# Kernel tuning notes

Hardware: AMD Instinct MI355X
Metric: run time of the kernel (lower is better)

Reference implementation:

```python
import jax, jax.numpy as jnp
import numpy as np

QMIN, QMAX = 0.0, 255.0  # uint8 affine quantization range


def _quant_dequant(x, scale, zero_point):
    # affine static quantization: q = clamp(round(x/scale) + zp, 0, 255)
    q = jnp.clip(jnp.round(x / scale) + zero_point, QMIN, QMAX)
    # dequantize back to float for the reference GEMM
    return (q - zero_point) * scale


def setup_inputs() -> dict:
    key = jax.random.key(0)
    k1, k2, k3, k4, k5 = jax.random.split(key, 5)
    N, IN, OUT = 4096, 4096, 4096
    x = jax.random.normal(k1, (N, IN), dtype=jnp.float32)
    weight = jax.random.normal(k2, (OUT, IN), dtype=jnp.float32) * 0.02
    bias = jax.random.normal(k3, (OUT,), dtype=jnp.float32)
    # static qparams (as produced by calculate_qparams of the observers)
    act_scale = jnp.float32(4.0 * 2.0 / 255.0)  # covers ~[-4, 4]
    act_zero_point = jnp.int32(128)
    weight_scale = (jax.random.uniform(k4, (OUT,), dtype=jnp.float32) * 0.5 + 0.5) * (0.08 * 2.0 / 255.0)
    weight_zero_point = jnp.full((OUT,), 128, dtype=jnp.int32)
    return {
        "x": x,
        "weight": weight,
        "bias": bias,
        "act_scale": act_scale,
        "act_zero_point": act_zero_point,
        "weight_scale": weight_scale,
        "weight_zero_point": weight_zero_point,
    }


def reference(x, weight, bias, act_scale, act_zero_point, weight_scale, weight_zero_point):
    # per-tensor static activation quantization
    x_dq = _quant_dequant(x, act_scale, act_zero_point.astype(jnp.float32))  # [N, in]
    # per-output-row weight quantization (block_size = (1, in_features))
    w_dq = _quant_dequant(
        weight,
        weight_scale[:, None],
        weight_zero_point.astype(jnp.float32)[:, None],
    )  # [out, in]
    # F.linear: x @ W^T + b
    return jnp.einsum("ni,oi->no", x_dq, w_dq) + bias
```

## Files before the change

### kernel.cpp

```cpp
#include <hip/hip_runtime.h>
#include <stdint.h>

typedef int   int4v   __attribute__((ext_vector_type(4)));
typedef float float4v __attribute__((ext_vector_type(4)));

static constexpr int DIM = 4096;
static constexpr int BM  = 256, BN = 256;
static constexpr int BK  = 128;
static constexpr int NKT = DIM / BK;

__global__ __launch_bounds__(256) void quant_act_kernel(
    const float* __restrict__ x, const float* __restrict__ s_ptr,
    const int* __restrict__ zp_ptr, int* __restrict__ out, int n4) {
  const float s  = s_ptr[0];
  const int   zp = zp_ptr[0];
  int idx    = blockIdx.x * blockDim.x + threadIdx.x;
  int stride = gridDim.x * blockDim.x;
  for (int i = idx; i < n4; i += stride) {
    float4v v = reinterpret_cast<const float4v*>(x)[i];
    int packed = 0;
#pragma unroll
    for (int j = 0; j < 4; ++j) {
      int q = (int)rintf(v[j] / s) + zp;
      q = min(max(q, 0), 255);
      q -= zp;
      packed |= (q & 255) << (8 * j);
    }
    out[i] = packed;
  }
}

__global__ __launch_bounds__(256) void quant_wgt_kernel(
    const float* __restrict__ w, const float* __restrict__ ws,
    const int* __restrict__ wzp, int* __restrict__ out, int n4) {
  int idx    = blockIdx.x * blockDim.x + threadIdx.x;
  int stride = gridDim.x * blockDim.x;
  for (int i = idx; i < n4; i += stride) {
    const int row = i >> 10;
    const float s = ws[row];
    const int  zp = wzp[row];
    float4v v = reinterpret_cast<const float4v*>(w)[i];
    int packed = 0;
#pragma unroll
    for (int j = 0; j < 4; ++j) {
      int q = (int)rintf(v[j] / s) + zp;
      q = min(max(q, 0), 255);
      q -= zp;
      packed |= (q & 255) << (8 * j);
    }
    out[i] = packed;
  }
}


#define PHASE_MFMA(MH, NH)                                                    \
  __builtin_amdgcn_s_barrier();                                               \
  asm volatile("s_waitcnt lgkmcnt(0)" ::: "memory");                          \
  __builtin_amdgcn_s_setprio(1);                                              \
  _Pragma("unroll") for (int kk = 0; kk < 2; ++kk)                            \
  _Pragma("unroll") for (int m = 0; m < 4; ++m)                               \
  _Pragma("unroll") for (int n = 0; n < 2; ++n)                               \
      acc[(MH)*4 + m][(NH)*2 + n] = __builtin_amdgcn_mfma_i32_16x16x64_i8(    \
          af[m][kk], bf[(NH)*2 + n][kk], acc[(MH)*4 + m][(NH)*2 + n], 0,0,0); \
  __builtin_amdgcn_s_setprio(0);                                              \
  __builtin_amdgcn_s_barrier();

__global__ __launch_bounds__(512) void gemm_i8_8ph(
    const signed char* __restrict__ A, const signed char* __restrict__ B,
    const float* __restrict__ s_act, const float* __restrict__ w_scale,
    const float* __restrict__ bias, float* __restrict__ C) {
  extern __shared__ signed char smem[];

  const int tid  = threadIdx.x;
  const int w    = tid >> 6;
  const int lane = tid & 63;
  const int wr = w >> 2, wc = w & 3;
  const int l15 = lane & 15, lhi = lane >> 4;
  const int swk = (l15 & 7) << 4;

  const int srow = lane >> 3;
  const int scol = ((lane & 7) ^ (lane >> 3)) << 4;

  const int tileM = blockIdx.y * BM;
  const int tileN = blockIdx.x * BN;

  auto stageA = [&](int i, int ktn, signed char* aL) {
    const int c = 4 * w + i;
    const size_t g = (size_t)(tileM + c * 8 + srow) * DIM + (size_t)ktn * BK + scol;
    __builtin_amdgcn_global_load_lds(
        (const __attribute__((address_space(1))) void*)(A + g),
        (__attribute__((address_space(3))) void*)(aL + c * 1024), 16, 0, 0);
  };
  auto stageB = [&](int i, int ktn, signed char* bL) {
    const int c = 4 * w + i;
    const size_t g = (size_t)(tileN + c * 8 + srow) * DIM + (size_t)ktn * BK + scol;
    __builtin_amdgcn_global_load_lds(
        (const __attribute__((address_space(1))) void*)(B + g),
        (__attribute__((address_space(3))) void*)(bL + c * 1024), 16, 0, 0);
  };
  auto rdA = [&](const signed char* aL, int mh, int m, int kk) -> int4v {
    const int r = wr * 128 + (mh * 4 + m) * 16 + l15;
    return *(const int4v*)(aL + r * BK + ((kk * 64 + lhi * 16) ^ swk));
  };
  auto rdB = [&](const signed char* bL, int nidx, int kk) -> int4v {
    const int r = wc * 64 + nidx * 16 + l15;
    return *(const int4v*)(bL + r * BK + ((kk * 64 + lhi * 16) ^ swk));
  };

  int4v acc[8][4] = {};
  int4v af[4][2];
  int4v bf[4][2];

  {
    signed char* aL = smem;
    signed char* bL = smem + 32768;
#pragma unroll
    for (int i = 0; i < 4; ++i) { stageA(i, 0, aL); stageB(i, 0, bL); }
  }
  asm volatile("s_waitcnt vmcnt(0)" ::: "memory");
  __builtin_amdgcn_s_barrier();

  for (int kt = 0; kt < NKT; ++kt) {
    signed char* aL = smem + (kt & 1) * 65536;
    signed char* bL = aL + 32768;
    signed char* aN = smem + ((kt + 1) & 1) * 65536;
    signed char* bN = aN + 32768;
    const int ktn = (kt + 1 < NKT) ? kt + 1 : kt;

#pragma unroll
    for (int m = 0; m < 4; ++m) { af[m][0] = rdA(aL, 0, m, 0); af[m][1] = rdA(aL, 0, m, 1); }
#pragma unroll
    for (int n = 0; n < 2; ++n) { bf[n][0] = rdB(bL, n, 0); bf[n][1] = rdB(bL, n, 1); }
    stageA(0, ktn, aN); stageA(1, ktn, aN); stageA(2, ktn, aN);
    PHASE_MFMA(0, 0)

#pragma unroll
    for (int n = 2; n < 4; ++n) { bf[n][0] = rdB(bL, n, 0); bf[n][1] = rdB(bL, n, 1); }
    stageA(3, ktn, aN); stageB(0, ktn, bN); stageB(1, ktn, bN);
    PHASE_MFMA(0, 1)

#pragma unroll
    for (int m = 0; m < 4; ++m) { af[m][0] = rdA(aL, 1, m, 0); af[m][1] = rdA(aL, 1, m, 1); }
    stageB(2, ktn, bN); stageB(3, ktn, bN);
    PHASE_MFMA(1, 0)

    __builtin_amdgcn_s_setprio(1);
#pragma unroll
    for (int kk = 0; kk < 2; ++kk)
#pragma unroll
      for (int m = 0; m < 4; ++m)
#pragma unroll
        for (int n = 0; n < 2; ++n)
          acc[4 + m][2 + n] = __builtin_amdgcn_mfma_i32_16x16x64_i8(
              af[m][kk], bf[2 + n][kk], acc[4 + m][2 + n], 0, 0, 0);
    __builtin_amdgcn_s_setprio(0);
    asm volatile("s_waitcnt vmcnt(0)" ::: "memory");
    __builtin_amdgcn_s_barrier();
  }

  const float sa = s_act[0];
#pragma unroll
  for (int n = 0; n < 4; ++n) {
    const int col = tileN + wc * 64 + n * 16 + l15;
    const float sc = sa * w_scale[col];
    const float bs = bias[col];
#pragma unroll
    for (int m = 0; m < 8; ++m) {
      const int rbase = tileM + wr * 128 + m * 16 + lhi * 4;
#pragma unroll
      for (int j = 0; j < 4; ++j)
        C[(size_t)(rbase + j) * DIM + col] = (float)acc[m][n][j] * sc + bs;
    }
  }
}

extern "C" void kernel_launch(void* const* d_in, const int* in_sizes, int n_in,
                              void* d_out, int out_size, void* d_ws, size_t ws_size,
                              hipStream_t stream) {
  const float* x    = (const float*)d_in[0];
  const float* w    = (const float*)d_in[1];
  const float* bias = (const float*)d_in[2];
  const float* a_s  = (const float*)d_in[3];
  const int*   a_zp = (const int*)d_in[4];
  const float* w_s  = (const float*)d_in[5];
  const int*   w_zp = (const int*)d_in[6];
  float* out = (float*)d_out;

  signed char* a8 = (signed char*)d_ws;
  signed char* b8 = a8 + (size_t)DIM * DIM;

  const int n4 = DIM * DIM / 4;
  quant_act_kernel<<<2048, 256, 0, stream>>>(x, a_s, a_zp, (int*)a8, n4);
  quant_wgt_kernel<<<2048, 256, 0, stream>>>(w, w_s, w_zp, (int*)b8, n4);

  (void)hipFuncSetAttribute((const void*)gemm_i8_8ph,
                            hipFuncAttributeMaxDynamicSharedMemorySize, 131072);
  dim3 grid(DIM / BN, DIM / BM);
  gemm_i8_8ph<<<grid, 512, 131072, stream>>>(a8, b8, a_s, w_s, bias, out);
}
```

Before: 97.28 us.

## Deepen GEMM global-to-LDS prefetch to two tiles and swizzle blocks across XCDs

The int8 GEMM now preloads two K tiles before the loop. It then refills the buffer just consumed with tile kt+2, waiting on vmcnt(8) instead of draining all loads. This gives global loads a full iteration of lead time to hide memory latency. The 2D grid becomes a 1D grid whose block index is remapped so that consecutive tiles of the same rows and columns land on the same XCD, which should improve L2 reuse of A and B. The refill is now issued in one burst after the third phase rather than spread across phases, which may cause bursty memory traffic.

```diff
diff --git a/kernel.cpp b/kernel.cpp
--- a/kernel.cpp
+++ b/kernel.cpp
@@ -81,8 +81,10 @@
   const int srow = lane >> 3;
   const int scol = ((lane & 7) ^ (lane >> 3)) << 4;
 
-  const int tileM = blockIdx.y * BM;
-  const int tileN = blockIdx.x * BN;
+  const int bid = blockIdx.x;
+  const int swz = (bid & 7) * 32 + (bid >> 3);
+  const int tileM = (swz >> 4) * BM;
+  const int tileN = (swz & 15) * BN;
 
   auto stageA = [&](int i, int ktn, signed char* aL) {
     const int c = 4 * w + i;
@@ -112,38 +114,41 @@
   int4v bf[4][2];
 
   {
-    signed char* aL = smem;
-    signed char* bL = smem + 32768;
-#pragma unroll
-    for (int i = 0; i < 4; ++i) { stageA(i, 0, aL); stageB(i, 0, bL); }
-  }
-  asm volatile("s_waitcnt vmcnt(0)" ::: "memory");
+    signed char* a0 = smem;
+    signed char* b0 = smem + 32768;
+    signed char* a1 = smem + 65536;
+    signed char* b1 = smem + 65536 + 32768;
+#pragma unroll
+    for (int i = 0; i < 4; ++i) { stageA(i, 0, a0); stageB(i, 0, b0); }
+#pragma unroll
+    for (int i = 0; i < 4; ++i) { stageA(i, 1, a1); stageB(i, 1, b1); }
+  }
+  asm volatile("s_waitcnt vmcnt(8)" ::: "memory");
   __builtin_amdgcn_s_barrier();
 
   for (int kt = 0; kt < NKT; ++kt) {
     signed char* aL = smem + (kt & 1) * 65536;
     signed char* bL = aL + 32768;
-    signed char* aN = smem + ((kt + 1) & 1) * 65536;
-    signed char* bN = aN + 32768;
-    const int ktn = (kt + 1 < NKT) ? kt + 1 : kt;
 
 #pragma unroll
     for (int m = 0; m < 4; ++m) { af[m][0] = rdA(aL, 0, m, 0); af[m][1] = rdA(aL, 0, m, 1); }
 #pragma unroll
     for (int n = 0; n < 2; ++n) { bf[n][0] = rdB(bL, n, 0); bf[n][1] = rdB(bL, n, 1); }
-    stageA(0, ktn, aN); stageA(1, ktn, aN); stageA(2, ktn, aN);
     PHASE_MFMA(0, 0)
 
 #pragma unroll
     for (int n = 2; n < 4; ++n) { bf[n][0] = rdB(bL, n, 0); bf[n][1] = rdB(bL, n, 1); }
-    stageA(3, ktn, aN); stageB(0, ktn, bN); stageB(1, ktn, bN);
     PHASE_MFMA(0, 1)
 
 #pragma unroll
     for (int m = 0; m < 4; ++m) { af[m][0] = rdA(aL, 1, m, 0); af[m][1] = rdA(aL, 1, m, 1); }
-    stageB(2, ktn, bN); stageB(3, ktn, bN);
     PHASE_MFMA(1, 0)
 
+    const bool st = (kt + 2 < NKT);
+    if (st) {
+#pragma unroll
+      for (int i = 0; i < 4; ++i) { stageA(i, kt + 2, aL); stageB(i, kt + 2, bL); }
+    }
     __builtin_amdgcn_s_setprio(1);
 #pragma unroll
     for (int kk = 0; kk < 2; ++kk)
@@ -154,7 +159,11 @@
           acc[4 + m][2 + n] = __builtin_amdgcn_mfma_i32_16x16x64_i8(
               af[m][kk], bf[2 + n][kk], acc[4 + m][2 + n], 0, 0, 0);
     __builtin_amdgcn_s_setprio(0);
-    asm volatile("s_waitcnt vmcnt(0)" ::: "memory");
+    if (st) {
+      asm volatile("s_waitcnt vmcnt(8)" ::: "memory");
+    } else {
+      asm volatile("s_waitcnt vmcnt(0)" ::: "memory");
+    }
     __builtin_amdgcn_s_barrier();
   }
 
@@ -195,6 +204,5 @@
 
   (void)hipFuncSetAttribute((const void*)gemm_i8_8ph,
                             hipFuncAttributeMaxDynamicSharedMemorySize, 131072);
-  dim3 grid(DIM / BN, DIM / BM);
-  gemm_i8_8ph<<<grid, 512, 131072, stream>>>(a8, b8, a_s, w_s, bias, out);
-}
+  gemm_i8_8ph<<<256, 512, 131072, stream>>>(a8, b8, a_s, w_s, bias, out);
+}
```

After: 99.21 us. No clear change (+2.0%).
